# Optimization experiments

Hardware: AMD Instinct MI355X
Metric: run time of the kernel (lower is better)

## Reference

```python
import jax, jax.numpy as jnp
import numpy as np

DIM_IN, DIM_OUT, DIM_INNER = 1024, 1024, 512

def setup_inputs() -> dict:
    key = jax.random.key(0)
    k1, k2, k3, k4 = jax.random.split(key, 4)
    x = jax.random.normal(k1, (4, 2048, DIM_IN), dtype=jnp.float32)
    # nn.Linear weights stored as [out, in]; init ~ U(-1/sqrt(in), 1/sqrt(in))
    w_qkv = jax.random.uniform(k2, (DIM_INNER * 3, DIM_IN), dtype=jnp.float32,
                               minval=-1.0, maxval=1.0) / np.sqrt(DIM_IN)
    w_out = jax.random.uniform(k3, (DIM_OUT, DIM_INNER), dtype=jnp.float32,
                               minval=-1.0, maxval=1.0) / np.sqrt(DIM_INNER)
    b_out = jax.random.uniform(k4, (DIM_OUT,), dtype=jnp.float32,
                               minval=-1.0, maxval=1.0) / np.sqrt(DIM_INNER)
    return {"x": x, "w_qkv": w_qkv, "w_out": w_out, "b_out": b_out}

def reference(x, w_qkv, w_out, b_out):
    scale = DIM_INNER ** -0.5
    qkv = jnp.einsum('bnd,ed->bne', x, w_qkv)  # [b, n, 3*dim_inner]
    q, k, v = jnp.split(qkv, 3, axis=-1)
    sim = jnp.einsum('bid,bjd->bij', q, k) * scale
    n = sim.shape[-1]
    causal = jnp.tril(jnp.ones((n, n), dtype=bool))  # True = keep
    sim = jnp.where(causal[None], sim, -jnp.finfo(sim.dtype).max)
    attn = jax.nn.softmax(sim, axis=-1)
    out = jnp.einsum('bij,bjd->bid', attn, v)
    return jnp.einsum('bnd,od->bno', out, w_out) + b_out
```

## Files before the change

### kernel.cpp

```cpp
#include <hip/hip_runtime.h>
#include <math.h>


typedef __attribute__((ext_vector_type(8))) short bf16x8_t;
typedef __attribute__((ext_vector_type(4))) float f32x4_t;

__device__ __forceinline__ unsigned short f2bf(float f) {
  unsigned int u = __float_as_uint(f);
  u = (u + 0x7FFFu + ((u >> 16) & 1u)) >> 16;
  return (unsigned short)u;
}
__device__ __forceinline__ float bf2f(unsigned short h) {
  return __uint_as_float(((unsigned int)h) << 16);
}

template <int N>
__device__ __forceinline__ void wait_vmcnt() {
  if constexpr (N == 0) asm volatile("s_waitcnt vmcnt(0)" ::: "memory");
  else if constexpr (N == 3) asm volatile("s_waitcnt vmcnt(3)" ::: "memory");
  else if constexpr (N == 4) asm volatile("s_waitcnt vmcnt(4)" ::: "memory");
  else if constexpr (N == 5) asm volatile("s_waitcnt vmcnt(5)" ::: "memory");
  else if constexpr (N == 6) asm volatile("s_waitcnt vmcnt(6)" ::: "memory");
}

__global__ __launch_bounds__(256) void cvt_all(
    const float* __restrict__ x, unsigned short* __restrict__ xb, int nx,
    const float* __restrict__ w1, unsigned short* __restrict__ w1b, int n1,
    const float* __restrict__ w2, unsigned short* __restrict__ w2b, int n2) {
  const int stride = gridDim.x * blockDim.x * 4;
  const int t0 = (blockIdx.x * blockDim.x + threadIdx.x) * 4;
  for (int i = t0; i < nx; i += stride) {
    float4 f = *(const float4*)(x + i);
    ushort4 u;
    u.x = f2bf(f.x); u.y = f2bf(f.y); u.z = f2bf(f.z); u.w = f2bf(f.w);
    *(ushort4*)(xb + i) = u;
  }
  for (int i = t0; i < n1; i += stride) {
    float4 f = *(const float4*)(w1 + i);
    ushort4 u;
    u.x = f2bf(f.x); u.y = f2bf(f.y); u.z = f2bf(f.z); u.w = f2bf(f.w);
    *(ushort4*)(w1b + i) = u;
  }
  for (int i = t0; i < n2; i += stride) {
    float4 f = *(const float4*)(w2 + i);
    ushort4 u;
    u.x = f2bf(f.x); u.y = f2bf(f.y); u.z = f2bf(f.z); u.w = f2bf(f.w);
    *(ushort4*)(w2b + i) = u;
  }
}

__global__ __launch_bounds__(256) void transpose_v(const unsigned short* __restrict__ src,
                                                   unsigned short* __restrict__ dst) {
  __shared__ unsigned short t[64][66];
  const int n0 = blockIdx.x * 64, e0 = blockIdx.y * 64;
  const unsigned short* s = src + (size_t)blockIdx.z * 2048 * 512;
  unsigned short* d = dst + (size_t)blockIdx.z * 512 * 2048;
  const int tc = threadIdx.x & 15;
  const int tr = threadIdx.x >> 4;
#pragma unroll
  for (int rr = 0; rr < 64; rr += 16) {
    ushort4 u = *(const ushort4*)(s + (size_t)(n0 + tr + rr) * 512 + e0 + tc * 4);
    t[tr + rr][tc * 4 + 0] = u.x;
    t[tr + rr][tc * 4 + 1] = u.y;
    t[tr + rr][tc * 4 + 2] = u.z;
    t[tr + rr][tc * 4 + 3] = u.w;
  }
  __syncthreads();
#pragma unroll
  for (int rr = 0; rr < 64; rr += 16) {
    ushort4 u;
    u.x = t[tc * 4 + 0][tr + rr];
    u.y = t[tc * 4 + 1][tr + rr];
    u.z = t[tc * 4 + 2][tr + rr];
    u.w = t[tc * 4 + 3][tr + rr];
    *(ushort4*)(d + (size_t)(e0 + tr + rr) * 2048 + n0 + tc * 4) = u;
  }
}

__global__ __launch_bounds__(256) void softmax_causal(unsigned short* __restrict__ sim) {
  const int lane = threadIdx.x & 63;
  const int rowg = blockIdx.x * 4 + (threadIdx.x >> 6);
  const int i = rowg & 2047;
  unsigned short* row = sim + (size_t)rowg * 2048;
  const int nv = i + 1;
  const int tb = ((i >> 7) + 1) << 7;
  const int nc = (nv + 255) >> 8;
  const int ns = (tb + 255) >> 8;

  float v[32];
  float m = -1e30f;
#pragma unroll
  for (int c = 0; c < 8; ++c) {
    if (c < nc) {
      const int j0 = c * 256 + lane * 4;
      ushort4 u = *(const ushort4*)(row + j0);
      float f0 = bf2f(u.x), f1 = bf2f(u.y), f2 = bf2f(u.z), f3 = bf2f(u.w);
      v[c * 4 + 0] = (j0 + 0 < nv) ? f0 : -1e30f;
      v[c * 4 + 1] = (j0 + 1 < nv) ? f1 : -1e30f;
      v[c * 4 + 2] = (j0 + 2 < nv) ? f2 : -1e30f;
      v[c * 4 + 3] = (j0 + 3 < nv) ? f3 : -1e30f;
      m = fmaxf(m, fmaxf(fmaxf(v[c * 4], v[c * 4 + 1]), fmaxf(v[c * 4 + 2], v[c * 4 + 3])));
    }
  }
#pragma unroll
  for (int s = 32; s >= 1; s >>= 1) m = fmaxf(m, __shfl_xor(m, s));
  float sum = 0.f;
#pragma unroll
  for (int c = 0; c < 8; ++c) {
    if (c < nc) {
#pragma unroll
      for (int e = 0; e < 4; ++e) {
        float p = __expf(v[c * 4 + e] - m);
        v[c * 4 + e] = p;
        sum += p;
      }
    }
  }
#pragma unroll
  for (int s = 32; s >= 1; s >>= 1) sum += __shfl_xor(sum, s);
  const float inv = 1.0f / sum;
#pragma unroll
  for (int c = 0; c < 8; ++c) {
    if (c < ns) {
      const int j0 = c * 256 + lane * 4;
      ushort4 u;
      if (c < nc) {
        u.x = f2bf(v[c * 4 + 0] * inv);
        u.y = f2bf(v[c * 4 + 1] * inv);
        u.z = f2bf(v[c * 4 + 2] * inv);
        u.w = f2bf(v[c * 4 + 3] * inv);
      } else {
        u.x = u.y = u.z = u.w = 0;
      }
      *(ushort4*)(row + j0) = u;
    }
  }
}

template <int EPI, int BM, int BN>
__global__ __launch_bounds__(256) void gemm_bt(
    const unsigned short* __restrict__ A, const unsigned short* __restrict__ B,
    int M, int N, int K, long strideA, long strideB, int klim, int causal,
    void* __restrict__ O0, void* __restrict__ O1, void* __restrict__ O2,
    const float* __restrict__ bias, float qscale) {
  const int bm = blockIdx.x, bn = blockIdx.y, bz = blockIdx.z;
  if (causal && bn > bm) return;
  const int tid = threadIdx.x, lane = tid & 63, wave = tid >> 6;
  const int wr = wave >> 1, wc = wave & 1;
  constexpr int FM = BM / 32, FN = BN / 32;
  constexpr int AR = BM / 64, BR = BN / 64;
  constexpr int L = AR + BR;

  __shared__ alignas(16) unsigned short As[3][BM * 32];
  __shared__ alignas(16) unsigned short Bs[3][BN * 32];

  const unsigned short* Ab = A + (size_t)bz * strideA + (size_t)bm * BM * K;
  const unsigned short* Bb = B + (size_t)bz * strideB + (size_t)bn * BN * K;

  const int kmax = klim ? min(K, (bm + 1) * BM) : K;
  const int nkt = kmax >> 5;

  auto stage = [&](int buf, int kt) {
    const int loff = tid * 16;
#pragma unroll
    for (int i = 0; i < AR; ++i) {
      const int o = i * 4096 + loff;
      const int r = o >> 6;
      const int sl = ((o >> 4) & 3) ^ ((r >> 1) & 3);
      __builtin_amdgcn_global_load_lds(
          (const __attribute__((address_space(1))) void*)(
              (const char*)(Ab + (size_t)r * K) + (size_t)kt * 64 + sl * 16),
          (__attribute__((address_space(3))) void*)((char*)As[buf] + o), 16, 0, 0);
    }
#pragma unroll
    for (int i = 0; i < BR; ++i) {
      const int o = i * 4096 + loff;
      const int r = o >> 6;
      const int sl = ((o >> 4) & 3) ^ ((r >> 1) & 3);
      __builtin_amdgcn_global_load_lds(
          (const __attribute__((address_space(1))) void*)(
              (const char*)(Bb + (size_t)r * K) + (size_t)kt * 64 + sl * 16),
          (__attribute__((address_space(3))) void*)((char*)Bs[buf] + o), 16, 0, 0);
    }
  };

  f32x4_t acc[FM][FN] = {};

  stage(0, 0);
  if (nkt > 1) stage(1, 1);
  int cur = 0;
  for (int kt = 0; kt < nkt; ++kt) {
    if (kt + 1 < nkt) wait_vmcnt<L>();
    else wait_vmcnt<0>();
    __builtin_amdgcn_s_barrier();

    bf16x8_t av[FM], bv[FN];
#pragma unroll
    for (int f = 0; f < FM; ++f) {
      const int row = wr * (BM / 2) + f * 16 + (lane & 15);
      const int sp = (lane >> 4) ^ ((row >> 1) & 3);
      av[f] = *(const bf16x8_t*)((const char*)As[cur] + row * 64 + sp * 16);
    }
#pragma unroll
    for (int f = 0; f < FN; ++f) {
      const int row = wc * (BN / 2) + f * 16 + (lane & 15);
      const int sp = (lane >> 4) ^ ((row >> 1) & 3);
      bv[f] = *(const bf16x8_t*)((const char*)Bs[cur] + row * 64 + sp * 16);
    }
    if (kt + 2 < nkt) {
      int nb = cur + 2;
      if (nb >= 3) nb -= 3;
      stage(nb, kt + 2);
    }
    asm volatile("s_waitcnt lgkmcnt(0)" ::: "memory");
    __builtin_amdgcn_sched_barrier(0);
    __builtin_amdgcn_s_setprio(1);
#pragma unroll
    for (int fi = 0; fi < FM; ++fi)
#pragma unroll
      for (int fj = 0; fj < FN; ++fj)
        acc[fi][fj] = __builtin_amdgcn_mfma_f32_16x16x32_bf16(av[fi], bv[fj], acc[fi][fj], 0, 0, 0);
    __builtin_amdgcn_s_setprio(0);
    __builtin_amdgcn_sched_barrier(0);
    cur = (cur + 1 == 3) ? 0 : cur + 1;
  }

#pragma unroll
  for (int fi = 0; fi < FM; ++fi) {
    const int row_l = wr * (BM / 2) + fi * 16 + ((lane >> 4) << 2);
#pragma unroll
    for (int fj = 0; fj < FN; ++fj) {
      const int col = bn * BN + wc * (BN / 2) + fj * 16 + (lane & 15);
#pragma unroll
      for (int r = 0; r < 4; ++r) {
        const int row = bm * BM + row_l + r;
        float v = acc[fi][fj][r];
        if constexpr (EPI == 0) {
          if (col < 512)
            ((unsigned short*)O0)[(size_t)row * 512 + col] = f2bf(v * qscale);
          else if (col < 1024)
            ((unsigned short*)O1)[(size_t)row * 512 + (col - 512)] = f2bf(v);
          else
            ((unsigned short*)O2)[(size_t)row * 512 + (col - 1024)] = f2bf(v);
        } else if constexpr (EPI == 1) {
          ((unsigned short*)O0)[(size_t)bz * 2048 * 2048 + (size_t)row * 2048 + col] = f2bf(v);
        } else if constexpr (EPI == 2) {
          ((unsigned short*)O0)[(size_t)bz * 2048 * 512 + (size_t)row * 512 + col] = f2bf(v);
        } else {
          ((float*)O0)[(size_t)row * 1024 + col] = v + bias[col];
        }
      }
    }
  }
}

extern "C" void kernel_launch(void* const* d_in, const int* in_sizes, int n_in,
                              void* d_out, int out_size, void* d_ws, size_t ws_size,
                              hipStream_t stream) {
  const float* x = (const float*)d_in[0];
  const float* w_qkv = (const float*)d_in[1];
  const float* w_out = (const float*)d_in[2];
  const float* b_out = (const float*)d_in[3];
  float* out = (float*)d_out;

  char* ws = (char*)d_ws;
  size_t off = 0;
  auto alloc = [&](size_t bytes) {
    size_t o = off;
    off += (bytes + 255) & ~(size_t)255;
    return o;
  };
  unsigned short* xb = (unsigned short*)(ws + alloc((size_t)8192 * 1024 * 2));
  unsigned short* wqkvb = (unsigned short*)(ws + alloc((size_t)1536 * 1024 * 2));
  unsigned short* woutb = (unsigned short*)(ws + alloc((size_t)1024 * 512 * 2));
  unsigned short* qb = (unsigned short*)(ws + alloc((size_t)8192 * 512 * 2));
  unsigned short* kb = (unsigned short*)(ws + alloc((size_t)8192 * 512 * 2));
  unsigned short* vb = (unsigned short*)(ws + alloc((size_t)8192 * 512 * 2));
  unsigned short* vtb = (unsigned short*)(ws + alloc((size_t)8192 * 512 * 2));
  unsigned short* sim = (unsigned short*)(ws + alloc((size_t)4 * 2048 * 2048 * 2));
  unsigned short* ao = (unsigned short*)(ws + alloc((size_t)8192 * 512 * 2));

  const float scale = 1.0f / sqrtf(512.0f);

  cvt_all<<<2048, 256, 0, stream>>>(x, xb, 8192 * 1024, w_qkv, wqkvb, 1536 * 1024,
                                    w_out, woutb, 1024 * 512);

  gemm_bt<0, 128, 192><<<dim3(64, 8, 1), 256, 0, stream>>>(
      xb, wqkvb, 8192, 1536, 1024, 0, 0, 0, 0, qb, kb, vb, nullptr, scale);

  transpose_v<<<dim3(32, 8, 4), 256, 0, stream>>>(vb, vtb);

  gemm_bt<1, 128, 128><<<dim3(16, 16, 4), 256, 0, stream>>>(
      qb, kb, 2048, 2048, 512, (long)2048 * 512, (long)2048 * 512,
      0, 1, sim, nullptr, nullptr, nullptr, 0.f);

  softmax_causal<<<2048, 256, 0, stream>>>(sim);

  gemm_bt<2, 128, 64><<<dim3(16, 8, 4), 256, 0, stream>>>(
      sim, vtb, 2048, 512, 2048, (long)2048 * 2048, (long)512 * 2048,
      1, 0, ao, nullptr, nullptr, nullptr, 0.f);

  gemm_bt<3, 128, 128><<<dim3(64, 8, 1), 256, 0, stream>>>(
      ao, woutb, 8192, 1024, 512, 0, 0, 0, 0, out, nullptr, nullptr, b_out, 0.f);
}
```

Baseline: 136.6 us.

## Fuse V transpose into QKV GEMM epilogue and switch to double buffering

The QKV projection epilogue now writes V straight into transposed [b, e, n] layout with 4-element vector stores, which removes the separate transpose_v kernel and the intermediate V buffer. The QKV GEMM tile changes from 128x192 to 128x128 (grid 64x12). The GEMM pipeline drops from a 3-stage to a 2-stage LDS ring, waiting on vmcnt(0) each iteration. That frees LDS and may raise occupancy, but it exposes more load latency since only one tile is prefetched ahead.

```diff
diff --git a/kernel.cpp b/kernel.cpp
--- a/kernel.cpp
+++ b/kernel.cpp
@@ -12,15 +12,6 @@
 }
 __device__ __forceinline__ float bf2f(unsigned short h) {
   return __uint_as_float(((unsigned int)h) << 16);
-}
-
-template <int N>
-__device__ __forceinline__ void wait_vmcnt() {
-  if constexpr (N == 0) asm volatile("s_waitcnt vmcnt(0)" ::: "memory");
-  else if constexpr (N == 3) asm volatile("s_waitcnt vmcnt(3)" ::: "memory");
-  else if constexpr (N == 4) asm volatile("s_waitcnt vmcnt(4)" ::: "memory");
-  else if constexpr (N == 5) asm volatile("s_waitcnt vmcnt(5)" ::: "memory");
-  else if constexpr (N == 6) asm volatile("s_waitcnt vmcnt(6)" ::: "memory");
 }
 
 __global__ __launch_bounds__(256) void cvt_all(
@@ -46,34 +37,6 @@
     ushort4 u;
     u.x = f2bf(f.x); u.y = f2bf(f.y); u.z = f2bf(f.z); u.w = f2bf(f.w);
     *(ushort4*)(w2b + i) = u;
-  }
-}
-
-__global__ __launch_bounds__(256) void transpose_v(const unsigned short* __restrict__ src,
-                                                   unsigned short* __restrict__ dst) {
-  __shared__ unsigned short t[64][66];
-  const int n0 = blockIdx.x * 64, e0 = blockIdx.y * 64;
-  const unsigned short* s = src + (size_t)blockIdx.z * 2048 * 512;
-  unsigned short* d = dst + (size_t)blockIdx.z * 512 * 2048;
-  const int tc = threadIdx.x & 15;
-  const int tr = threadIdx.x >> 4;
-#pragma unroll
-  for (int rr = 0; rr < 64; rr += 16) {
-    ushort4 u = *(const ushort4*)(s + (size_t)(n0 + tr + rr) * 512 + e0 + tc * 4);
-    t[tr + rr][tc * 4 + 0] = u.x;
-    t[tr + rr][tc * 4 + 1] = u.y;
-    t[tr + rr][tc * 4 + 2] = u.z;
-    t[tr + rr][tc * 4 + 3] = u.w;
-  }
-  __syncthreads();
-#pragma unroll
-  for (int rr = 0; rr < 64; rr += 16) {
-    ushort4 u;
-    u.x = t[tc * 4 + 0][tr + rr];
-    u.y = t[tc * 4 + 1][tr + rr];
-    u.z = t[tc * 4 + 2][tr + rr];
-    u.w = t[tc * 4 + 3][tr + rr];
-    *(ushort4*)(d + (size_t)(e0 + tr + rr) * 2048 + n0 + tc * 4) = u;
   }
 }
 
@@ -149,10 +112,9 @@
   const int wr = wave >> 1, wc = wave & 1;
   constexpr int FM = BM / 32, FN = BN / 32;
   constexpr int AR = BM / 64, BR = BN / 64;
-  constexpr int L = AR + BR;
-
-  __shared__ alignas(16) unsigned short As[3][BM * 32];
-  __shared__ alignas(16) unsigned short Bs[3][BN * 32];
+
+  __shared__ alignas(16) unsigned short As[2][BM * 32];
+  __shared__ alignas(16) unsigned short Bs[2][BN * 32];
 
   const unsigned short* Ab = A + (size_t)bz * strideA + (size_t)bm * BM * K;
   const unsigned short* Bb = B + (size_t)bz * strideB + (size_t)bn * BN * K;
@@ -187,12 +149,11 @@
   f32x4_t acc[FM][FN] = {};
 
   stage(0, 0);
-  if (nkt > 1) stage(1, 1);
-  int cur = 0;
   for (int kt = 0; kt < nkt; ++kt) {
-    if (kt + 1 < nkt) wait_vmcnt<L>();
-    else wait_vmcnt<0>();
+    const int cur = kt & 1;
+    asm volatile("s_waitcnt vmcnt(0)" ::: "memory");
     __builtin_amdgcn_s_barrier();
+    if (kt + 1 < nkt) stage(cur ^ 1, kt + 1);
 
     bf16x8_t av[FM], bv[FN];
 #pragma unroll
@@ -207,11 +168,6 @@
       const int sp = (lane >> 4) ^ ((row >> 1) & 3);
       bv[f] = *(const bf16x8_t*)((const char*)Bs[cur] + row * 64 + sp * 16);
     }
-    if (kt + 2 < nkt) {
-      int nb = cur + 2;
-      if (nb >= 3) nb -= 3;
-      stage(nb, kt + 2);
-    }
     asm volatile("s_waitcnt lgkmcnt(0)" ::: "memory");
     __builtin_amdgcn_sched_barrier(0);
     __builtin_amdgcn_s_setprio(1);
@@ -222,7 +178,6 @@
         acc[fi][fj] = __builtin_amdgcn_mfma_f32_16x16x32_bf16(av[fi], bv[fj], acc[fi][fj], 0, 0, 0);
     __builtin_amdgcn_s_setprio(0);
     __builtin_amdgcn_sched_barrier(0);
-    cur = (cur + 1 == 3) ? 0 : cur + 1;
   }
 
 #pragma unroll
@@ -231,23 +186,40 @@
 #pragma unroll
     for (int fj = 0; fj < FN; ++fj) {
       const int col = bn * BN + wc * (BN / 2) + fj * 16 + (lane & 15);
-#pragma unroll
-      for (int r = 0; r < 4; ++r) {
-        const int row = bm * BM + row_l + r;
-        float v = acc[fi][fj][r];
-        if constexpr (EPI == 0) {
-          if (col < 512)
-            ((unsigned short*)O0)[(size_t)row * 512 + col] = f2bf(v * qscale);
-          else if (col < 1024)
-            ((unsigned short*)O1)[(size_t)row * 512 + (col - 512)] = f2bf(v);
-          else
-            ((unsigned short*)O2)[(size_t)row * 512 + (col - 1024)] = f2bf(v);
-        } else if constexpr (EPI == 1) {
-          ((unsigned short*)O0)[(size_t)bz * 2048 * 2048 + (size_t)row * 2048 + col] = f2bf(v);
-        } else if constexpr (EPI == 2) {
-          ((unsigned short*)O0)[(size_t)bz * 2048 * 512 + (size_t)row * 512 + col] = f2bf(v);
+      if constexpr (EPI == 0) {
+        const int row0 = bm * BM + row_l;
+        if (col < 512) {
+#pragma unroll
+          for (int r = 0; r < 4; ++r)
+            ((unsigned short*)O0)[(size_t)(row0 + r) * 512 + col] =
+                f2bf(acc[fi][fj][r] * qscale);
+        } else if (col < 1024) {
+#pragma unroll
+          for (int r = 0; r < 4; ++r)
+            ((unsigned short*)O1)[(size_t)(row0 + r) * 512 + (col - 512)] =
+                f2bf(acc[fi][fj][r]);
         } else {
-          ((float*)O0)[(size_t)row * 1024 + col] = v + bias[col];
+          const int e = col - 1024;
+          const int b = row0 >> 11, n0 = row0 & 2047;
+          ushort4 u;
+          u.x = f2bf(acc[fi][fj][0]);
+          u.y = f2bf(acc[fi][fj][1]);
+          u.z = f2bf(acc[fi][fj][2]);
+          u.w = f2bf(acc[fi][fj][3]);
+          *(ushort4*)((unsigned short*)O2 + ((size_t)b * 512 + e) * 2048 + n0) = u;
+        }
+      } else {
+#pragma unroll
+        for (int r = 0; r < 4; ++r) {
+          const int row = bm * BM + row_l + r;
+          float v = acc[fi][fj][r];
+          if constexpr (EPI == 1) {
+            ((unsigned short*)O0)[(size_t)bz * 2048 * 2048 + (size_t)row * 2048 + col] = f2bf(v);
+          } else if constexpr (EPI == 2) {
+            ((unsigned short*)O0)[(size_t)bz * 2048 * 512 + (size_t)row * 512 + col] = f2bf(v);
+          } else {
+            ((float*)O0)[(size_t)row * 1024 + col] = v + bias[col];
+          }
         }
       }
     }
@@ -275,7 +247,6 @@
   unsigned short* woutb = (unsigned short*)(ws + alloc((size_t)1024 * 512 * 2));
   unsigned short* qb = (unsigned short*)(ws + alloc((size_t)8192 * 512 * 2));
   unsigned short* kb = (unsigned short*)(ws + alloc((size_t)8192 * 512 * 2));
-  unsigned short* vb = (unsigned short*)(ws + alloc((size_t)8192 * 512 * 2));
   unsigned short* vtb = (unsigned short*)(ws + alloc((size_t)8192 * 512 * 2));
   unsigned short* sim = (unsigned short*)(ws + alloc((size_t)4 * 2048 * 2048 * 2));
   unsigned short* ao = (unsigned short*)(ws + alloc((size_t)8192 * 512 * 2));
@@ -285,10 +256,8 @@
   cvt_all<<<2048, 256, 0, stream>>>(x, xb, 8192 * 1024, w_qkv, wqkvb, 1536 * 1024,
                                     w_out, woutb, 1024 * 512);
 
-  gemm_bt<0, 128, 192><<<dim3(64, 8, 1), 256, 0, stream>>>(
-      xb, wqkvb, 8192, 1536, 1024, 0, 0, 0, 0, qb, kb, vb, nullptr, scale);
-
-  transpose_v<<<dim3(32, 8, 4), 256, 0, stream>>>(vb, vtb);
+  gemm_bt<0, 128, 128><<<dim3(64, 12, 1), 256, 0, stream>>>(
+      xb, wqkvb, 8192, 1536, 1024, 0, 0, 0, 0, qb, kb, vtb, nullptr, scale);
 
   gemm_bt<1, 128, 128><<<dim3(16, 16, 4), 256, 0, stream>>>(
       qb, kb, 2048, 2048, 512, (long)2048 * 512, (long)2048 * 512,
```

Result: slower. 141.2 us (+3.4%).
